# Kernel optimization log

Hardware: AMD Instinct MI355X
Metric: run time of the kernel (lower is better)

## Reference

```python
import jax, jax.numpy as jnp
import numpy as np

N_NODES = 100000
N_EDGES = 6400000
PENALTY_N = 0.1  # init arg `n`


def setup_inputs() -> dict:
    key = jax.random.key(0)
    k1, k2, k3, k4, k5 = jax.random.split(key, 5)
    edge_index = jax.random.randint(k1, (2, N_EDGES), 0, N_NODES, dtype=jnp.int64 if jax.config.read('jax_enable_x64') else jnp.int32)
    edge_weight = jax.random.uniform(k2, (N_EDGES,), dtype=jnp.float32)
    nodes_yield_rate = jax.random.uniform(k3, (N_NODES,), dtype=jnp.float32)
    nodes_traffic = jax.random.uniform(k4, (N_NODES,), dtype=jnp.float32)
    nodes_cost = jax.random.uniform(k5, (N_NODES,), dtype=jnp.float32)
    return {
        'edge_index': edge_index,
        'edge_weight': edge_weight,
        'nodes_yield_rate': nodes_yield_rate,
        'nodes_traffic': nodes_traffic,
        'nodes_cost': nodes_cost,
    }


def reference(edge_index, edge_weight, nodes_yield_rate, nodes_traffic, nodes_cost):
    # Original loop reads src/dst traffic from the ORIGINAL tensor and accumulates
    # updates into a clone; both branches are equivalent to:
    #   src -= |diff| * n * w ; dst += |diff| * n * w
    # i.e. a pure per-edge scatter-add with no edge-order dependency.
    src = edge_index[0]
    dst = edge_index[1]
    diff = nodes_traffic[src] - nodes_traffic[dst]          # [E]
    transfer = jnp.abs(diff) * PENALTY_N * edge_weight      # [E]
    new_traffic = nodes_traffic.at[src].add(-transfer).at[dst].add(transfer)
    total_service_efficiency = jnp.sum(nodes_yield_rate * new_traffic - nodes_cost)
    return new_traffic, total_service_efficiency
```

## Files before the change

kernel.cpp:

```cpp
#include <hip/hip_runtime.h>

#define PENALTY_N 0.1f
#define CP 20000
#define MAX_BPP 102
#define ABLK 1024

__global__ __launch_bounds__(ABLK, 8) void part_scatter_kernel(
    const int* __restrict__ src_idx,
    const int* __restrict__ dst_idx,
    const float* __restrict__ w,
    const float* __restrict__ traffic,
    float* __restrict__ scratch,
    float* __restrict__ out_scalar,
    int nE, int nN, int Bpp) {
    __shared__ float hist[CP];

    const int p = blockIdx.x / Bpp;
    const int b = blockIdx.x % Bpp;
    const int lo = p * CP;
    const unsigned csz = (unsigned)min(CP, nN - lo);
    const int tid = threadIdx.x;

    if (blockIdx.x == 0 && tid == 0) *out_scalar = 0.0f;

    for (int i = tid; i < CP; i += ABLK) hist[i] = 0.0f;
    __syncthreads();

    const int nvec = nE >> 2;
    const int4* __restrict__ src4 = (const int4*)src_idx;
    const int4* __restrict__ dst4 = (const int4*)dst_idx;
    const float4* __restrict__ w4 = (const float4*)w;
    const int stride = Bpp * ABLK;

    for (int v = b * ABLK + tid; v < nvec; v += stride) {
        int4 s = src4[v];
        int4 d = dst4[v];
        float4 ww = w4[v];

        #pragma unroll
        for (int k = 0; k < 4; ++k) {
            int si = (&s.x)[k];
            int di = (&d.x)[k];
            unsigned so = (unsigned)(si - lo);
            unsigned doo = (unsigned)(di - lo);
            bool inS = so < csz;
            bool inD = doo < csz;
            if (inS || inD) {
                float t = fabsf(traffic[si] - traffic[di]) * (PENALTY_N * (&ww.x)[k]);
                if (inS) atomicAdd(&hist[so], -t);
                if (inD) atomicAdd(&hist[doo], t);
            }
        }
    }
    for (int e = (nvec << 2) + b * ABLK + tid; e < nE; e += stride) {
        int si = src_idx[e];
        int di = dst_idx[e];
        unsigned so = (unsigned)(si - lo);
        unsigned doo = (unsigned)(di - lo);
        bool inS = so < csz;
        bool inD = doo < csz;
        if (inS || inD) {
            float t = fabsf(traffic[si] - traffic[di]) * (PENALTY_N * w[e]);
            if (inS) atomicAdd(&hist[so], -t);
            if (inD) atomicAdd(&hist[doo], t);
        }
    }

    __syncthreads();
    float* dst = scratch + (size_t)blockIdx.x * CP;
    for (int i = tid; i < CP; i += ABLK) dst[i] = hist[i];
}

__global__ __launch_bounds__(256) void part_reduce_kernel(
    const float* __restrict__ scratch,
    const float* __restrict__ traffic,
    const float* __restrict__ yield_rate,
    const float* __restrict__ cost,
    float* __restrict__ out,
    int nN, int Bpp) {
    const int tid = blockIdx.x * blockDim.x + threadIdx.x;
    const int stride = gridDim.x * blockDim.x;

    float acc = 0.0f;
    for (int i = tid; i < nN; i += stride) {
        int p = i / CP;
        int off = i - p * CP;
        const float* base = scratch + ((size_t)p * Bpp + 0) * CP + off;

        float s0 = traffic[i], s1 = 0.0f, s2 = 0.0f, s3 = 0.0f;
        int b = 0;
        for (; b + 8 <= Bpp; b += 8) {
            const float* q = base + (size_t)b * CP;
            float a0 = q[0 * (size_t)CP];
            float a1 = q[1 * (size_t)CP];
            float a2 = q[2 * (size_t)CP];
            float a3 = q[3 * (size_t)CP];
            float a4 = q[4 * (size_t)CP];
            float a5 = q[5 * (size_t)CP];
            float a6 = q[6 * (size_t)CP];
            float a7 = q[7 * (size_t)CP];
            s0 += a0 + a4;
            s1 += a1 + a5;
            s2 += a2 + a6;
            s3 += a3 + a7;
        }
        for (; b < Bpp; ++b) s0 += base[(size_t)b * CP];
        float s = (s0 + s1) + (s2 + s3);
        out[i] = s;
        acc = fmaf(yield_rate[i], s, acc) - cost[i];
    }

    #pragma unroll
    for (int off = 32; off > 0; off >>= 1) acc += __shfl_down(acc, off, 64);

    __shared__ float wsum[4];
    const int lane = threadIdx.x & 63;
    const int wid = threadIdx.x >> 6;
    if (lane == 0) wsum[wid] = acc;
    __syncthreads();
    if (threadIdx.x == 0)
        atomicAdd(&out[nN], wsum[0] + wsum[1] + wsum[2] + wsum[3]);
}

__global__ void init_out_kernel(const float* __restrict__ traffic,
                                float* __restrict__ out, int nN) {
    int i = blockIdx.x * blockDim.x + threadIdx.x;
    if (i < nN) out[i] = traffic[i];
    else if (i == nN) out[i] = 0.0f;
}

__global__ __launch_bounds__(256) void edge_scatter_kernel(
    const int* __restrict__ src_idx, const int* __restrict__ dst_idx,
    const float* __restrict__ w, const float* __restrict__ traffic,
    float* __restrict__ out, int nE) {
    const int tid = blockIdx.x * blockDim.x + threadIdx.x;
    const int stride = gridDim.x * blockDim.x;
    for (int e = tid; e < nE; e += stride) {
        int s = src_idx[e];
        int d = dst_idx[e];
        float t = fabsf(traffic[s] - traffic[d]) * (PENALTY_N * w[e]);
        atomicAdd(&out[s], -t);
        atomicAdd(&out[d], t);
    }
}

__global__ __launch_bounds__(256) void reduce_kernel(
    const float* __restrict__ new_traffic, const float* __restrict__ yield_rate,
    const float* __restrict__ cost, float* __restrict__ total, int nN) {
    const int tid = blockIdx.x * blockDim.x + threadIdx.x;
    const int stride = gridDim.x * blockDim.x;
    float acc = 0.0f;
    for (int i = tid; i < nN; i += stride)
        acc = fmaf(yield_rate[i], new_traffic[i], acc) - cost[i];
    #pragma unroll
    for (int off = 32; off > 0; off >>= 1) acc += __shfl_down(acc, off, 64);
    __shared__ float wsum[4];
    const int lane = threadIdx.x & 63;
    const int wid = threadIdx.x >> 6;
    if (lane == 0) wsum[wid] = acc;
    __syncthreads();
    if (threadIdx.x == 0)
        atomicAdd(total, wsum[0] + wsum[1] + wsum[2] + wsum[3]);
}

extern "C" void kernel_launch(void* const* d_in, const int* in_sizes, int n_in,
                              void* d_out, int out_size, void* d_ws, size_t ws_size,
                              hipStream_t stream) {
    const int* edge_index = (const int*)d_in[0];
    const float* edge_weight = (const float*)d_in[1];
    const float* nodes_yield = (const float*)d_in[2];
    const float* nodes_traffic = (const float*)d_in[3];
    const float* nodes_cost = (const float*)d_in[4];
    float* out = (float*)d_out;

    const int nE = in_sizes[1];
    const int nN = in_sizes[2];
    const int* src_idx = edge_index;
    const int* dst_idx = edge_index + nE;

    const int P = (nN + CP - 1) / CP;
    int Bpp = (int)(ws_size / ((size_t)P * CP * sizeof(float)));
    if (Bpp > MAX_BPP) Bpp = MAX_BPP;

    if (Bpp >= 4 && P <= 8) {
        float* scratch = (float*)d_ws;
        part_scatter_kernel<<<P * Bpp, ABLK, 0, stream>>>(
            src_idx, dst_idx, edge_weight, nodes_traffic,
            scratch, out + nN, nE, nN, Bpp);
        int rgrid = (nN + 255) / 256;
        part_reduce_kernel<<<rgrid, 256, 0, stream>>>(
            scratch, nodes_traffic, nodes_yield, nodes_cost, out, nN, Bpp);
    } else {
        int grid = (nN + 1 + 255) / 256;
        init_out_kernel<<<grid, 256, 0, stream>>>(nodes_traffic, out, nN);
        edge_scatter_kernel<<<2048, 256, 0, stream>>>(src_idx, dst_idx,
                                                      edge_weight, nodes_traffic,
                                                      out, nE);
        reduce_kernel<<<256, 256, 0, stream>>>(out, nodes_yield, nodes_cost,
                                               out + nN, nN);
    }
}
```

Measured before the change: 229.3 us.

## Enlarge LDS histogram partitions, use branchless dummy-slot atomics, vectorize init/flush

Each block's LDS histogram partition grows from 20000 to 33344 nodes, so the 100k nodes fit in 3 partitions instead of 5. Every partition re-reads the whole edge list, so fewer partitions means fewer full passes over edges. Out-of-range endpoints now send their atomic to a padded dummy slot instead of branching. The histogram zeroing and the copy-out to scratch use float4. In exchange, LDS per block rises to about 133KB, which lowers occupancy (launch bounds change from 8 to 4). Blocks per partition drop to 85, which adds more atomics per block and wasted dummy atomics.

```diff
diff --git a/kernel.cpp b/kernel.cpp
--- a/kernel.cpp
+++ b/kernel.cpp
@@ -1,11 +1,12 @@
 #include <hip/hip_runtime.h>
 
 #define PENALTY_N 0.1f
-#define CP 20000
-#define MAX_BPP 102
+#define CP 33344
+#define HPAD 64
+#define MAX_BPP 85
 #define ABLK 1024
 
-__global__ __launch_bounds__(ABLK, 8) void part_scatter_kernel(
+__global__ __launch_bounds__(ABLK, 4) void part_scatter_kernel(
     const int* __restrict__ src_idx,
     const int* __restrict__ dst_idx,
     const float* __restrict__ w,
@@ -13,7 +14,7 @@
     float* __restrict__ scratch,
     float* __restrict__ out_scalar,
     int nE, int nN, int Bpp) {
-    __shared__ float hist[CP];
+    __shared__ float hist[CP + HPAD];
 
     const int p = blockIdx.x / Bpp;
     const int b = blockIdx.x % Bpp;
@@ -23,7 +24,12 @@
 
     if (blockIdx.x == 0 && tid == 0) *out_scalar = 0.0f;
 
-    for (int i = tid; i < CP; i += ABLK) hist[i] = 0.0f;
+    {
+        float4* h4 = (float4*)hist;
+        const int n4 = (CP + HPAD) / 4;
+        for (int i = tid; i < n4; i += ABLK)
+            h4[i] = make_float4(0.f, 0.f, 0.f, 0.f);
+    }
     __syncthreads();
 
     const int nvec = nE >> 2;
@@ -47,8 +53,10 @@
             bool inD = doo < csz;
             if (inS || inD) {
                 float t = fabsf(traffic[si] - traffic[di]) * (PENALTY_N * (&ww.x)[k]);
-                if (inS) atomicAdd(&hist[so], -t);
-                if (inD) atomicAdd(&hist[doo], t);
+                unsigned iS = inS ? so : (unsigned)CP;
+                unsigned iD = inD ? doo : (unsigned)CP;
+                atomicAdd(&hist[iS], -t);
+                atomicAdd(&hist[iD], t);
             }
         }
     }
@@ -61,14 +69,22 @@
         bool inD = doo < csz;
         if (inS || inD) {
             float t = fabsf(traffic[si] - traffic[di]) * (PENALTY_N * w[e]);
-            if (inS) atomicAdd(&hist[so], -t);
-            if (inD) atomicAdd(&hist[doo], t);
+            unsigned iS = inS ? so : (unsigned)CP;
+            unsigned iD = inD ? doo : (unsigned)CP;
+            atomicAdd(&hist[iS], -t);
+            atomicAdd(&hist[iD], t);
         }
     }
 
     __syncthreads();
     float* dst = scratch + (size_t)blockIdx.x * CP;
-    for (int i = tid; i < CP; i += ABLK) dst[i] = hist[i];
+    {
+        const int n4 = (int)(csz >> 2);
+        float4* d4 = (float4*)dst;
+        const float4* h4 = (const float4*)hist;
+        for (int i = tid; i < n4; i += ABLK) d4[i] = h4[i];
+        for (int i = (n4 << 2) + tid; i < (int)csz; i += ABLK) dst[i] = hist[i];
+    }
 }
 
 __global__ __launch_bounds__(256) void part_reduce_kernel(
@@ -85,7 +101,7 @@
     for (int i = tid; i < nN; i += stride) {
         int p = i / CP;
         int off = i - p * CP;
-        const float* base = scratch + ((size_t)p * Bpp + 0) * CP + off;
+        const float* base = scratch + (size_t)p * Bpp * CP + off;
 
         float s0 = traffic[i], s1 = 0.0f, s2 = 0.0f, s3 = 0.0f;
         int b = 0;
```

New measurement: 227.4 us. Within noise of the previous version (-0.8%).
